# Performance work log

Measured on AMD Instinct MI355X. Metric: run time of the kernel, lower is better.

Reference implementation:

```python
import jax, jax.numpy as jnp
import numpy as np

MASK_SCALE = 0.05


def setup_inputs() -> dict:
    key = jax.random.key(0)
    k1, k2, k3 = jax.random.split(key, 3)
    B, S, H = 4, 2048, 4096
    OUT = (32 + 2 * 8) * 128  # (num_heads + 2*num_kv_heads) * head_size = 6144
    x = jax.random.normal(k1, (B, S, H), dtype=jnp.float32)
    weight = jax.random.normal(k2, (OUT, H), dtype=jnp.float32) * (H ** -0.5)
    # noise pool sample r ~ noise_scale * N(0,1), shape [hidden_size]
    r = jax.random.normal(k3, (H,), dtype=jnp.float32) * MASK_SCALE
    return {"x": x, "weight": weight, "r": r}


def reference(x, weight, r):
    # Encrypt: subtract broadcast mask along hidden dim.
    x_masked = x - r  # [B,S,H] - [H]
    # GEMM on masked input (untrusted-side compute): y_masked = x_masked @ W^T
    y_masked = jnp.einsum("bsh,oh->bso", x_masked, weight)
    # Decrypt: add precomputed rW = W @ r (NoisePool correction term).
    rw = weight @ r  # [OUT]
    y = y_masked + rw
    return y
```

## Files before the change

kernel.cpp:

```cpp
#include <hip/hip_runtime.h>
#include <hip/hip_bf16.h>
#include <hip/hip_fp16.h>


typedef __attribute__((ext_vector_type(8))) _Float16 f16x8;
typedef __attribute__((ext_vector_type(8))) short bf16x8;
typedef __attribute__((ext_vector_type(4))) float f32x4;
typedef __attribute__((ext_vector_type(4))) short s16x4;
typedef __attribute__((address_space(3))) void as3void;
typedef const __attribute__((address_space(1))) void as1void;

__global__ void convert_f16_tiled(const float* __restrict__ X, const float* __restrict__ W,
                                  _Float16* __restrict__ wsX, _Float16* __restrict__ wsW,
                                  int K, long tilesX, long tilesW) {
  const int lane = threadIdx.x & 63;
  const long wav = (long)blockIdx.x * (blockDim.x >> 6) + (threadIdx.x >> 6);
  const long nw = (long)gridDim.x * (blockDim.x >> 6);
  const int ko = lane >> 4, r16 = lane & 15;
  const long KT = K >> 5;
  const long total = tilesX + tilesW;
  for (long t = wav; t < total; t += nw) {
    const float* src; _Float16* dst; long tt;
    if (t < tilesX) { src = X; dst = wsX; tt = t; }
    else            { src = W; dst = wsW; tt = t - tilesX; }
    long rt = tt / KT, kt = tt - rt * KT;
    const float* p = src + (rt * 16 + r16) * (long)K + kt * 32 + ko * 8;
    float4 v0 = *reinterpret_cast<const float4*>(p);
    float4 v1 = *reinterpret_cast<const float4*>(p + 4);
    f16x8 h;
    h[0] = (_Float16)v0.x; h[1] = (_Float16)v0.y; h[2] = (_Float16)v0.z; h[3] = (_Float16)v0.w;
    h[4] = (_Float16)v1.x; h[5] = (_Float16)v1.y; h[6] = (_Float16)v1.z; h[7] = (_Float16)v1.w;
    *reinterpret_cast<f16x8*>(dst + tt * 512 + lane * 8) = h;
  }
}

#define GBM 256
#define GBN 256
#define GBK 64

__global__ __launch_bounds__(512, 2)
void qkv_gemm_f16(const _Float16* __restrict__ wsX, const _Float16* __restrict__ wsW,
                  float* __restrict__ Y, int M, int N, int K) {
  __shared__ __align__(16) _Float16 lds[65536];

  const int tid = threadIdx.x, lane = tid & 63, wid = tid >> 6;
  const int nbm = M / GBM, nbn = N / GBN;
  const int nwg = nbm * nbn;

  int bid = blockIdx.x, bm, bn;
  if ((nbn % 8 == 0) && (nwg % 8 == 0)) {
    int xcd = bid & 7, local = bid >> 3;
    bm = local % nbm;
    bn = xcd * (nbn / 8) + local / nbm;
  } else {
    bm = bid % nbm; bn = bid / nbm;
  }

  const long KT = K >> 5;
  const int bmrt = bm * (GBM / 16);
  const int bnrt = bn * (GBN / 16);

  auto STAGE = [&](int cur, int kt64) {
    const long k2 = (long)kt64 * 2;
    #pragma unroll
    for (int q = 0; q < 2; ++q) {
      const int i = wid * 2 + q;
      const _Float16* sA = wsX + ((bmrt + i) * KT + k2) * 512;
      const _Float16* sB = wsW + ((bnrt + i) * KT + k2) * 512;
      _Float16* dA = &lds[cur * 32768 + i * 1024];
      _Float16* dB = &lds[cur * 32768 + 16384 + i * 1024];
      #pragma unroll
      for (int s = 0; s < 2; ++s) {
        __builtin_amdgcn_global_load_lds((as1void*)(sA + s * 512 + lane * 8),
                                         (as3void*)(dA + s * 512), 16, 0, 0);
        __builtin_amdgcn_global_load_lds((as1void*)(sB + s * 512 + lane * 8),
                                         (as3void*)(dB + s * 512), 16, 0, 0);
      }
    }
  };

  const int wr = wid >> 2, wc = wid & 3;
  const int l15 = lane & 15, lk = lane >> 4;

  f32x4 acc[8][4];
  #pragma unroll
  for (int m = 0; m < 8; ++m)
    #pragma unroll
    for (int n = 0; n < 4; ++n) acc[m][n] = (f32x4){0.f, 0.f, 0.f, 0.f};

  auto COMPUTE = [&](int cur) {
    const _Float16* La = &lds[cur * 32768 + (wr * 8) * 1024 + lane * 8];
    const _Float16* Lb = &lds[cur * 32768 + 16384 + (wc * 4) * 1024 + lane * 8];
    #pragma unroll
    for (int s = 0; s < 2; ++s) {
      f16x8 b[4];
      #pragma unroll
      for (int n = 0; n < 4; ++n)
        b[n] = *reinterpret_cast<const f16x8*>(Lb + n * 1024 + s * 512);
      #pragma unroll
      for (int m = 0; m < 8; ++m) {
        f16x8 a = *reinterpret_cast<const f16x8*>(La + m * 1024 + s * 512);
        #pragma unroll
        for (int n = 0; n < 4; ++n)
          acc[m][n] = __builtin_amdgcn_mfma_f32_16x16x32_f16(a, b[n], acc[m][n], 0, 0, 0);
      }
    }
  };

  const int NK = K / GBK;
  STAGE(0, 0);
  int cur = 0;
  #pragma unroll 1
  for (int kt = 0; kt + 1 < NK; ++kt) {
    STAGE(cur ^ 1, kt + 1);
    __builtin_amdgcn_sched_barrier(0);
    asm volatile("s_waitcnt vmcnt(8)" ::: "memory");
    __builtin_amdgcn_sched_barrier(0);
    __builtin_amdgcn_s_barrier();
    __builtin_amdgcn_sched_barrier(0);
    COMPUTE(cur);
    __builtin_amdgcn_s_barrier();
    __builtin_amdgcn_sched_barrier(0);
    cur ^= 1;
  }
  __builtin_amdgcn_sched_barrier(0);
  asm volatile("s_waitcnt vmcnt(0)" ::: "memory");
  __builtin_amdgcn_sched_barrier(0);
  __builtin_amdgcn_s_barrier();
  __builtin_amdgcn_sched_barrier(0);
  COMPUTE(cur);

  const int brow = bm * GBM, bcol = bn * GBN;
  float* Yw = Y + (size_t)(brow + wr * 128) * N + bcol + wc * 64;
  #pragma unroll
  for (int m = 0; m < 8; ++m)
    #pragma unroll
    for (int n = 0; n < 4; ++n)
      #pragma unroll
      for (int j = 0; j < 4; ++j)
        Yw[(size_t)(m * 16 + lk * 4 + j) * N + n * 16 + l15] = acc[m][n][j];
}

#define FBM 128
#define FBN 128
#define FBK 32
#define FBKP 40

__device__ __forceinline__ unsigned short f2bf_hi(float f, float& hif) {
  unsigned u = __float_as_uint(f);
  unsigned r = (u + 0x7FFFu + ((u >> 16) & 1u)) & 0xFFFF0000u;
  hif = __uint_as_float(r);
  return (unsigned short)(r >> 16);
}
__device__ __forceinline__ unsigned short f2bf(float f) {
  unsigned u = __float_as_uint(f);
  return (unsigned short)((u + 0x7FFFu + ((u >> 16) & 1u)) >> 16);
}

__global__ __launch_bounds__(256, 2)
void qkv_gemm_split3(const float* __restrict__ X, const float* __restrict__ W,
                     float* __restrict__ Y, int M, int N, int K) {
  __shared__ __align__(16) short sAhi[FBM * FBKP];
  __shared__ __align__(16) short sAlo[FBM * FBKP];
  __shared__ __align__(16) short sBhi[FBN * FBKP];
  __shared__ __align__(16) short sBlo[FBN * FBKP];

  const int tid = threadIdx.x;
  const int nbm = M / FBM, nbn = N / FBN;
  const int nwg = nbm * nbn;
  int bid = blockIdx.x;
  int b2 = (bid & 7) * (nwg >> 3) + (bid >> 3);
  const int GRP = 8;
  int gsz = GRP * nbn;
  int g = b2 / gsz, rr = b2 % gsz;
  int bm = g * GRP + (rr & (GRP - 1));
  int bn = rr / GRP;

  const int brow = bm * FBM, bcol = bn * FBN;
  const float* Ab = X + (size_t)brow * K;
  const float* Bb = W + (size_t)bcol * K;
  const int srow = tid >> 3, sc4 = tid & 7;

  float4 curA[4], curB[4], nxtA[4], nxtB[4];
  auto issue = [&](float4* ra, float4* rb, int k0) {
    #pragma unroll
    for (int p = 0; p < 4; ++p) {
      int row = srow + p * 32;
      ra[p] = *reinterpret_cast<const float4*>(Ab + (size_t)row * K + k0 + sc4 * 4);
      rb[p] = *reinterpret_cast<const float4*>(Bb + (size_t)row * K + k0 + sc4 * 4);
    }
  };
  auto stage = [&](const float4* ra, const float4* rb) {
    #pragma unroll
    for (int p = 0; p < 4; ++p) {
      int row = srow + p * 32;
      int off = row * FBKP + sc4 * 4;
      float4 va = ra[p], vb = rb[p];
      s16x4 ahi, alo, bhi, blo;
      #pragma unroll
      for (int e = 0; e < 4; ++e) {
        float fa = (&va.x)[e], fb = (&vb.x)[e];
        float fah, fbh;
        ahi[e] = (short)f2bf_hi(fa, fah);
        alo[e] = (short)f2bf(fa - fah);
        bhi[e] = (short)f2bf_hi(fb, fbh);
        blo[e] = (short)f2bf(fb - fbh);
      }
      *reinterpret_cast<s16x4*>(&sAhi[off]) = ahi;
      *reinterpret_cast<s16x4*>(&sAlo[off]) = alo;
      *reinterpret_cast<s16x4*>(&sBhi[off]) = bhi;
      *reinterpret_cast<s16x4*>(&sBlo[off]) = blo;
    }
  };

  const int lane = tid & 63;
  const int wid = tid >> 6;
  const int wr = wid >> 1, wc = wid & 1;
  const int l15 = lane & 15, lk = lane >> 4;

  f32x4 acc[4][4];
  #pragma unroll
  for (int m = 0; m < 4; ++m)
    #pragma unroll
    for (int n = 0; n < 4; ++n) acc[m][n] = (f32x4){0.f, 0.f, 0.f, 0.f};

  const int aoff = (wr * 64 + l15) * FBKP + lk * 8;
  const int boff = (wc * 64 + l15) * FBKP + lk * 8;

  auto compute = [&]() {
    bf16x8 bhi[4], blo[4];
    #pragma unroll
    for (int n = 0; n < 4; ++n) {
      bhi[n] = *reinterpret_cast<const bf16x8*>(&sBhi[boff + n * 16 * FBKP]);
      blo[n] = *reinterpret_cast<const bf16x8*>(&sBlo[boff + n * 16 * FBKP]);
    }
    #pragma unroll
    for (int m = 0; m < 4; ++m) {
      bf16x8 ahi = *reinterpret_cast<const bf16x8*>(&sAhi[aoff + m * 16 * FBKP]);
      bf16x8 alo = *reinterpret_cast<const bf16x8*>(&sAlo[aoff + m * 16 * FBKP]);
      #pragma unroll
      for (int n = 0; n < 4; ++n) {
        acc[m][n] = __builtin_amdgcn_mfma_f32_16x16x32_bf16(alo, bhi[n], acc[m][n], 0, 0, 0);
        acc[m][n] = __builtin_amdgcn_mfma_f32_16x16x32_bf16(ahi, blo[n], acc[m][n], 0, 0, 0);
        acc[m][n] = __builtin_amdgcn_mfma_f32_16x16x32_bf16(ahi, bhi[n], acc[m][n], 0, 0, 0);
      }
    }
  };

  const int NK = K / FBK;
  issue(curA, curB, 0);
  #pragma unroll 1
  for (int kt = 0; kt < NK; kt += 2) {
    issue(nxtA, nxtB, (kt + 1) * FBK);
    stage(curA, curB);
    __syncthreads();
    compute();
    __syncthreads();
    if (kt + 2 < NK) issue(curA, curB, (kt + 2) * FBK);
    stage(nxtA, nxtB);
    __syncthreads();
    compute();
    __syncthreads();
  }

  float* Yw = Y + (size_t)(brow + wr * 64) * N + bcol + wc * 64;
  #pragma unroll
  for (int m = 0; m < 4; ++m)
    #pragma unroll
    for (int n = 0; n < 4; ++n)
      #pragma unroll
      for (int j = 0; j < 4; ++j)
        Yw[(size_t)(m * 16 + lk * 4 + j) * N + n * 16 + l15] = acc[m][n][j];
}

extern "C" void kernel_launch(void* const* d_in, const int* in_sizes, int n_in,
                              void* d_out, int out_size, void* d_ws, size_t ws_size,
                              hipStream_t stream) {
  const float* X = (const float*)d_in[0];
  const float* W = (const float*)d_in[1];
  float* Y = (float*)d_out;

  const int K = 4096;
  const int M = in_sizes[0] / K;
  const int N = in_sizes[1] / K;
  const long tilesX = ((long)M / 16) * (K / 32);
  const long tilesW = ((long)N / 16) * (K / 32);
  const size_t ws_needed = (size_t)((long)M * K + (long)N * K) * sizeof(_Float16);

  if (ws_size >= ws_needed) {
    _Float16* wsX = (_Float16*)d_ws;
    _Float16* wsW = wsX + (long)M * K;
    convert_f16_tiled<<<dim3(2048), dim3(256), 0, stream>>>(X, W, wsX, wsW, K, tilesX, tilesW);
    dim3 grid((M / GBM) * (N / GBN));
    qkv_gemm_f16<<<grid, dim3(512), 0, stream>>>(wsX, wsW, Y, M, N, K);
  } else {
    dim3 grid((M / FBM) * (N / FBN));
    qkv_gemm_split3<<<grid, dim3(256), 0, stream>>>(X, W, Y, M, N, K);
  }
}
```

Baseline: 725.9 us.

## Deepen GEMM pipeline to 4-stage K=32 ring with split prefetch and setprio

The GEMM main loop moves from a two-buffer K=64 scheme to a four-buffer ring of K=32 tiles that keeps three tiles in flight. Each tile's loads and MFMA work are split into two halves with barriers, and s_setprio raises priority during the MFMA bursts. The f16 conversion kernel now stages 16x512 fp32 chunks through shared memory so global reads are row-contiguous. The XCD-aware block remap now groups blocks in 8x8 patches. This adds more barriers per K step and gates the fast path on shape divisibility.

```diff
diff --git a/kernel.cpp b/kernel.cpp
--- a/kernel.cpp
+++ b/kernel.cpp
@@ -10,33 +10,47 @@
 typedef __attribute__((address_space(3))) void as3void;
 typedef const __attribute__((address_space(1))) void as1void;
 
-__global__ void convert_f16_tiled(const float* __restrict__ X, const float* __restrict__ W,
-                                  _Float16* __restrict__ wsX, _Float16* __restrict__ wsW,
-                                  int K, long tilesX, long tilesW) {
-  const int lane = threadIdx.x & 63;
-  const long wav = (long)blockIdx.x * (blockDim.x >> 6) + (threadIdx.x >> 6);
-  const long nw = (long)gridDim.x * (blockDim.x >> 6);
-  const int ko = lane >> 4, r16 = lane & 15;
+__global__ __launch_bounds__(256)
+void convert_f16_t2(const float* __restrict__ X, const float* __restrict__ W,
+                    _Float16* __restrict__ wsX, _Float16* __restrict__ wsW,
+                    int K, int nbX) {
+  __shared__ float sb[16 * 516];
+  const int KC = K >> 9;
+  int bid = blockIdx.x;
+  const float* src; _Float16* dst; int rt, kc;
+  if (bid < nbX) { src = X; dst = wsX; rt = bid / KC; kc = bid % KC; }
+  else { int b2 = bid - nbX; src = W; dst = wsW; rt = b2 / KC; kc = b2 % KC; }
+
+  const int tid = threadIdx.x;
+  #pragma unroll
+  for (int i = 0; i < 8; ++i) {
+    int flat = i * 256 + tid;
+    int row = flat >> 7, c4 = flat & 127;
+    float4 v = *reinterpret_cast<const float4*>(
+        src + (size_t)(rt * 16 + row) * K + kc * 512 + c4 * 4);
+    *reinterpret_cast<float4*>(&sb[row * 516 + c4 * 4]) = v;
+  }
+  __syncthreads();
+
+  const int lane = tid & 63, w = tid >> 6;
+  const int r = lane & 15, ko = lane >> 4;
   const long KT = K >> 5;
-  const long total = tilesX + tilesW;
-  for (long t = wav; t < total; t += nw) {
-    const float* src; _Float16* dst; long tt;
-    if (t < tilesX) { src = X; dst = wsX; tt = t; }
-    else            { src = W; dst = wsW; tt = t - tilesX; }
-    long rt = tt / KT, kt = tt - rt * KT;
-    const float* p = src + (rt * 16 + r16) * (long)K + kt * 32 + ko * 8;
-    float4 v0 = *reinterpret_cast<const float4*>(p);
-    float4 v1 = *reinterpret_cast<const float4*>(p + 4);
+  #pragma unroll
+  for (int j = 0; j < 4; ++j) {
+    int lt = w * 4 + j;
+    const float* p = &sb[r * 516 + lt * 32 + ko * 8];
+    float4 f0 = *reinterpret_cast<const float4*>(p);
+    float4 f1 = *reinterpret_cast<const float4*>(p + 4);
     f16x8 h;
-    h[0] = (_Float16)v0.x; h[1] = (_Float16)v0.y; h[2] = (_Float16)v0.z; h[3] = (_Float16)v0.w;
-    h[4] = (_Float16)v1.x; h[5] = (_Float16)v1.y; h[6] = (_Float16)v1.z; h[7] = (_Float16)v1.w;
-    *reinterpret_cast<f16x8*>(dst + tt * 512 + lane * 8) = h;
+    h[0] = (_Float16)f0.x; h[1] = (_Float16)f0.y; h[2] = (_Float16)f0.z; h[3] = (_Float16)f0.w;
+    h[4] = (_Float16)f1.x; h[5] = (_Float16)f1.y; h[6] = (_Float16)f1.z; h[7] = (_Float16)f1.w;
+    *reinterpret_cast<f16x8*>(dst + ((size_t)rt * KT + kc * 16 + lt) * 512 + lane * 8) = h;
   }
 }
 
 #define GBM 256
 #define GBN 256
-#define GBK 64
+#define GBK 32
 
 __global__ __launch_bounds__(512, 2)
 void qkv_gemm_f16(const _Float16* __restrict__ wsX, const _Float16* __restrict__ wsW,
@@ -45,37 +59,36 @@
 
   const int tid = threadIdx.x, lane = tid & 63, wid = tid >> 6;
   const int nbm = M / GBM, nbn = N / GBN;
-  const int nwg = nbm * nbn;
 
   int bid = blockIdx.x, bm, bn;
-  if ((nbn % 8 == 0) && (nwg % 8 == 0)) {
+  if (nbm % 8 == 0 && nbn % 8 == 0) {
     int xcd = bid & 7, local = bid >> 3;
-    bm = local % nbm;
-    bn = xcd * (nbn / 8) + local / nbm;
-  } else {
-    bm = bid % nbm; bn = bid / nbm;
-  }
+    int nbnx = nbn / 8;
+    int span = 8 * nbnx;
+    int g = local / span, rr = local % span;
+    bm = g * 8 + (rr & 7);
+    bn = xcd * nbnx + (rr >> 3);
+  } else { bm = bid % nbm; bn = bid / nbm; }
 
   const long KT = K >> 5;
   const int bmrt = bm * (GBM / 16);
   const int bnrt = bn * (GBN / 16);
 
-  auto STAGE = [&](int cur, int kt64) {
-    const long k2 = (long)kt64 * 2;
-    #pragma unroll
-    for (int q = 0; q < 2; ++q) {
-      const int i = wid * 2 + q;
-      const _Float16* sA = wsX + ((bmrt + i) * KT + k2) * 512;
-      const _Float16* sB = wsW + ((bnrt + i) * KT + k2) * 512;
-      _Float16* dA = &lds[cur * 32768 + i * 1024];
-      _Float16* dB = &lds[cur * 32768 + 16384 + i * 1024];
-      #pragma unroll
-      for (int s = 0; s < 2; ++s) {
-        __builtin_amdgcn_global_load_lds((as1void*)(sA + s * 512 + lane * 8),
-                                         (as3void*)(dA + s * 512), 16, 0, 0);
-        __builtin_amdgcn_global_load_lds((as1void*)(sB + s * 512 + lane * 8),
-                                         (as3void*)(dB + s * 512), 16, 0, 0);
+  auto STAGE2 = [&](int t, int half) {
+    const int b = t & 3;
+    #pragma unroll
+    for (int j = 0; j < 2; ++j) {
+      const int c = wid * 4 + half * 2 + j;
+      const _Float16* src;
+      const _Float16* dstb;
+      if (c < 16) {
+        src = wsX + ((size_t)(bmrt + c) * KT + t) * 512 + lane * 8;
+        dstb = &lds[b * 16384 + c * 512];
+      } else {
+        src = wsW + ((size_t)(bnrt + (c - 16)) * KT + t) * 512 + lane * 8;
+        dstb = &lds[b * 16384 + 8192 + (c - 16) * 512];
       }
+      __builtin_amdgcn_global_load_lds((as1void*)src, (as3void*)dstb, 16, 0, 0);
     }
   };
 
@@ -88,47 +101,61 @@
     #pragma unroll
     for (int n = 0; n < 4; ++n) acc[m][n] = (f32x4){0.f, 0.f, 0.f, 0.f};
 
-  auto COMPUTE = [&](int cur) {
-    const _Float16* La = &lds[cur * 32768 + (wr * 8) * 1024 + lane * 8];
-    const _Float16* Lb = &lds[cur * 32768 + 16384 + (wc * 4) * 1024 + lane * 8];
-    #pragma unroll
-    for (int s = 0; s < 2; ++s) {
-      f16x8 b[4];
-      #pragma unroll
-      for (int n = 0; n < 4; ++n)
-        b[n] = *reinterpret_cast<const f16x8*>(Lb + n * 1024 + s * 512);
-      #pragma unroll
-      for (int m = 0; m < 8; ++m) {
-        f16x8 a = *reinterpret_cast<const f16x8*>(La + m * 1024 + s * 512);
-        #pragma unroll
-        for (int n = 0; n < 4; ++n)
-          acc[m][n] = __builtin_amdgcn_mfma_f32_16x16x32_f16(a, b[n], acc[m][n], 0, 0, 0);
-      }
-    }
-  };
-
   const int NK = K / GBK;
-  STAGE(0, 0);
-  int cur = 0;
-  #pragma unroll 1
-  for (int kt = 0; kt + 1 < NK; ++kt) {
-    STAGE(cur ^ 1, kt + 1);
-    __builtin_amdgcn_sched_barrier(0);
-    asm volatile("s_waitcnt vmcnt(8)" ::: "memory");
-    __builtin_amdgcn_sched_barrier(0);
-    __builtin_amdgcn_s_barrier();
-    __builtin_amdgcn_sched_barrier(0);
-    COMPUTE(cur);
-    __builtin_amdgcn_s_barrier();
-    __builtin_amdgcn_sched_barrier(0);
-    cur ^= 1;
-  }
-  __builtin_amdgcn_sched_barrier(0);
-  asm volatile("s_waitcnt vmcnt(0)" ::: "memory");
+
+  STAGE2(0, 0); STAGE2(0, 1);
+  STAGE2(1, 0); STAGE2(1, 1);
+  STAGE2(2, 0); STAGE2(2, 1);
+  asm volatile("s_waitcnt vmcnt(8)" ::: "memory");
   __builtin_amdgcn_sched_barrier(0);
   __builtin_amdgcn_s_barrier();
-  __builtin_amdgcn_sched_barrier(0);
-  COMPUTE(cur);
+
+#define GEMM_TILE(T, PF, VMSTR)                                              \
+  do {                                                                       \
+    const int b_ = (T) & 3;                                                  \
+    const _Float16* Ab_ = &lds[b_ * 16384 + wr * 4096 + lane * 8];           \
+    const _Float16* Bb_ = &lds[b_ * 16384 + 8192 + wc * 2048 + lane * 8];    \
+    f16x8 af[4], bf[4], af2[4];                                              \
+    _Pragma("unroll") for (int n = 0; n < 4; ++n)                            \
+        bf[n] = *reinterpret_cast<const f16x8*>(Bb_ + n * 512);              \
+    _Pragma("unroll") for (int m = 0; m < 4; ++m)                            \
+        af[m] = *reinterpret_cast<const f16x8*>(Ab_ + m * 512);              \
+    if (PF) STAGE2((T) + 3, 0);                                              \
+    __builtin_amdgcn_s_barrier();                                            \
+    asm volatile("s_waitcnt lgkmcnt(0)" ::: "memory");                       \
+    __builtin_amdgcn_sched_barrier(0);                                       \
+    __builtin_amdgcn_s_setprio(1);                                           \
+    _Pragma("unroll") for (int m = 0; m < 4; ++m)                            \
+        _Pragma("unroll") for (int n = 0; n < 4; ++n)                        \
+            acc[m][n] = __builtin_amdgcn_mfma_f32_16x16x32_f16(              \
+                af[m], bf[n], acc[m][n], 0, 0, 0);                           \
+    __builtin_amdgcn_s_setprio(0);                                           \
+    __builtin_amdgcn_s_barrier();                                            \
+    _Pragma("unroll") for (int m = 0; m < 4; ++m)                            \
+        af2[m] = *reinterpret_cast<const f16x8*>(Ab_ + (m + 4) * 512);       \
+    if (PF) STAGE2((T) + 3, 1);                                              \
+    asm volatile("s_waitcnt vmcnt(" VMSTR ")" ::: "memory");                 \
+    __builtin_amdgcn_sched_barrier(0);                                       \
+    __builtin_amdgcn_s_barrier();                                            \
+    asm volatile("s_waitcnt lgkmcnt(0)" ::: "memory");                       \
+    __builtin_amdgcn_sched_barrier(0);                                       \
+    __builtin_amdgcn_s_setprio(1);                                           \
+    _Pragma("unroll") for (int m = 0; m < 4; ++m)                            \
+        _Pragma("unroll") for (int n = 0; n < 4; ++n)                        \
+            acc[m + 4][n] = __builtin_amdgcn_mfma_f32_16x16x32_f16(          \
+                af2[m], bf[n], acc[m + 4][n], 0, 0, 0);                      \
+    __builtin_amdgcn_s_setprio(0);                                           \
+    __builtin_amdgcn_s_barrier();                                            \
+  } while (0)
+
+  #pragma unroll 1
+  for (int t = 0; t < NK - 3; ++t) {
+    GEMM_TILE(t, true, "8");
+  }
+  GEMM_TILE(NK - 3, false, "4");
+  GEMM_TILE(NK - 2, false, "0");
+  GEMM_TILE(NK - 1, false, "0");
+#undef GEMM_TILE
 
   const int brow = bm * GBM, bcol = bn * GBN;
   float* Yw = Y + (size_t)(brow + wr * 128) * N + bcol + wc * 64;
@@ -283,14 +310,14 @@
   const int K = 4096;
   const int M = in_sizes[0] / K;
   const int N = in_sizes[1] / K;
-  const long tilesX = ((long)M / 16) * (K / 32);
-  const long tilesW = ((long)N / 16) * (K / 32);
   const size_t ws_needed = (size_t)((long)M * K + (long)N * K) * sizeof(_Float16);
 
-  if (ws_size >= ws_needed) {
+  if (ws_size >= ws_needed && (M % 256) == 0 && (N % 256) == 0 && (K % 512) == 0) {
     _Float16* wsX = (_Float16*)d_ws;
     _Float16* wsW = wsX + (long)M * K;
-    convert_f16_tiled<<<dim3(2048), dim3(256), 0, stream>>>(X, W, wsX, wsW, K, tilesX, tilesW);
+    const int nbX = (M / 16) * (K / 512);
+    const int nbW = (N / 16) * (K / 512);
+    convert_f16_t2<<<dim3(nbX + nbW), dim3(256), 0, stream>>>(X, W, wsX, wsW, K, nbX);
     dim3 grid((M / GBM) * (N / GBN));
     qkv_gemm_f16<<<grid, dim3(512), 0, stream>>>(wsX, wsW, Y, M, N, K);
   } else {
```

New measurement: 715.7 us. Within noise of the previous version (-1.4%).
